# Kernel tuning notes

Measured on AMD Instinct MI355X. Metric: run time of the kernel, lower is better.

## Reference

```python
import jax, jax.numpy as jnp
import numpy as np

B, N, D = 2, 2048, 1024          # batch, query tokens, model dim
NC, DC = 77, 768                 # context tokens, context dim (CLIP)
H, DH = 16, 64                   # heads, head dim (H*DH == D)
FF = 4 * D                       # GEGLU inner dim
SCALE = DH ** -0.5
EPS = 1e-5


def setup_inputs() -> dict:
    key = jax.random.key(0)
    ks = iter(jax.random.split(key, 32))
    rn = lambda *s: jax.random.normal(next(ks), s, dtype=jnp.float32) * 0.02
    inp = {
        'x': jax.random.normal(next(ks), (B, N, D), dtype=jnp.float32),
        'context': jax.random.normal(next(ks), (B, NC, DC), dtype=jnp.float32),
        # attn1 (self-attention): all projections from dim D
        'w1_q': rn(D, D), 'w1_k': rn(D, D), 'w1_v': rn(D, D),
        'w1_o': rn(D, D), 'b1_o': jnp.zeros((D,), jnp.float32),
        # attn2 (cross-attention): k/v from context dim DC
        'w2_q': rn(D, D), 'w2_k': rn(DC, D), 'w2_v': rn(DC, D),
        'w2_o': rn(D, D), 'b2_o': jnp.zeros((D,), jnp.float32),
        # layernorms
        'ln1_g': jnp.ones((D,), jnp.float32), 'ln1_b': jnp.zeros((D,), jnp.float32),
        'ln2_g': jnp.ones((D,), jnp.float32), 'ln2_b': jnp.zeros((D,), jnp.float32),
        'ln3_g': jnp.ones((D,), jnp.float32), 'ln3_b': jnp.zeros((D,), jnp.float32),
        # GEGLU feed-forward: proj -> 2*FF (value, gate), then FF -> D
        'ff_w1': rn(D, 2 * FF), 'ff_b1': jnp.zeros((2 * FF,), jnp.float32),
        'ff_w2': rn(FF, D), 'ff_b2': jnp.zeros((D,), jnp.float32),
    }
    return inp


def _layer_norm(x, g, b):
    mu = jnp.mean(x, axis=-1, keepdims=True)
    var = jnp.mean(jnp.square(x - mu), axis=-1, keepdims=True)
    return (x - mu) * jax.lax.rsqrt(var + EPS) * g + b


def _attention(xq, ctx, wq, wk, wv, wo, bo):
    b, n, _ = xq.shape
    m = ctx.shape[1]
    q = (xq @ wq).reshape(b, n, H, DH)
    k = (ctx @ wk).reshape(b, m, H, DH)
    v = (ctx @ wv).reshape(b, m, H, DH)
    sim = jnp.einsum('bihd,bjhd->bhij', q, k) * SCALE
    attn = jax.nn.softmax(sim, axis=-1)
    out = jnp.einsum('bhij,bjhd->bihd', attn, v).reshape(b, n, H * DH)
    return out @ wo + bo


def reference(x, context,
              w1_q, w1_k, w1_v, w1_o, b1_o,
              w2_q, w2_k, w2_v, w2_o, b2_o,
              ln1_g, ln1_b, ln2_g, ln2_b, ln3_g, ln3_b,
              ff_w1, ff_b1, ff_w2, ff_b2):
    # self-attention + residual
    h = _layer_norm(x, ln1_g, ln1_b)
    x = _attention(h, h, w1_q, w1_k, w1_v, w1_o, b1_o) + x
    # cross-attention + residual
    h = _layer_norm(x, ln2_g, ln2_b)
    x = _attention(h, context, w2_q, w2_k, w2_v, w2_o, b2_o) + x
    # GEGLU feed-forward + residual (torch F.gelu is exact erf)
    h = _layer_norm(x, ln3_g, ln3_b)
    p = h @ ff_w1 + ff_b1
    val, gate = p[..., :FF], p[..., FF:]
    x = (val * jax.nn.gelu(gate, approximate=False)) @ ff_w2 + ff_b2 + x
    return x
```

## Files before the change

kernel.cpp:

```cpp
#include <hip/hip_runtime.h>
#include <hip/hip_bf16.h>
#include <math.h>

#define B_    2
#define N_    2048
#define D_    1024
#define NC_   77
#define DC_   768
#define H_    16
#define DH_   64
#define FF_   4096
#define EPS_  1e-5f
#define SCALE_ 0.125f
#define NEG_BIG -1e30f

typedef __attribute__((ext_vector_type(8))) short short8;
typedef __attribute__((ext_vector_type(4))) float f32x4;
#define MFMA16(a, b, c) __builtin_amdgcn_mfma_f32_16x16x32_bf16(a, b, c, 0, 0, 0)

static __device__ __forceinline__ unsigned short f2bf_raw(float f) {
    union { float f; unsigned int i; } x; x.f = f;
    unsigned int r = x.i + 0x7fffu + ((x.i >> 16) & 1u);
    return (unsigned short)(r >> 16);
}

static __device__ __forceinline__ void gload16(const void* g, void* l) {
    __builtin_amdgcn_global_load_lds(
        (const __attribute__((address_space(1))) void*)g,
        (__attribute__((address_space(3))) void*)l, 16, 0, 0);
}

__global__ __launch_bounds__(256) void wtrans_k(const float* __restrict__ src,
                                                unsigned short* __restrict__ dst,
                                                int K, int N) {
    __shared__ unsigned short t[64][68];
    const int k0 = blockIdx.y * 64, n0 = blockIdx.x * 64;
    const int rr = threadIdx.x >> 4;
    const int cc = (threadIdx.x & 15) * 4;
#pragma unroll
    for (int p = 0; p < 4; p++) {
        int k = rr + p * 16;
        float4 vd = *(const float4*)&src[(size_t)(k0 + k) * N + n0 + cc];
        t[k][cc + 0] = f2bf_raw(vd.x); t[k][cc + 1] = f2bf_raw(vd.y);
        t[k][cc + 2] = f2bf_raw(vd.z); t[k][cc + 3] = f2bf_raw(vd.w);
    }
    __syncthreads();
#pragma unroll
    for (int p = 0; p < 4; p++) {
        int n = rr + p * 16;
        ushort4 o;
        o.x = t[cc + 0][n]; o.y = t[cc + 1][n];
        o.z = t[cc + 2][n]; o.w = t[cc + 3][n];
        *(ushort4*)&dst[(size_t)(n0 + n) * K + k0 + cc] = o;
    }
}

__global__ __launch_bounds__(256) void ln_k(const float* __restrict__ x,
                                            const float* __restrict__ g,
                                            const float* __restrict__ b,
                                            unsigned short* __restrict__ out) {
    int row = blockIdx.x;
    const float* xr = x + (size_t)row * D_;
    float v0[4]; float s = 0.f, sq = 0.f;
#pragma unroll
    for (int i = 0; i < 4; i++) {
        float t = xr[threadIdx.x + 256 * i];
        v0[i] = t; s += t; sq += t * t;
    }
#pragma unroll
    for (int off = 32; off; off >>= 1) {
        s  += __shfl_xor(s,  off);
        sq += __shfl_xor(sq, off);
    }
    __shared__ float rs[4], rq[4];
    int wave = threadIdx.x >> 6, lane = threadIdx.x & 63;
    if (lane == 0) { rs[wave] = s; rq[wave] = sq; }
    __syncthreads();
    s  = rs[0] + rs[1] + rs[2] + rs[3];
    sq = rq[0] + rq[1] + rq[2] + rq[3];
    float mu  = s * (1.f / D_);
    float var = sq * (1.f / D_) - mu * mu;
    float inv = rsqrtf(var + EPS_);
#pragma unroll
    for (int i = 0; i < 4; i++) {
        int c = threadIdx.x + 256 * i;
        out[(size_t)row * D_ + c] = f2bf_raw((v0[i] - mu) * inv * g[c] + b[c]);
    }
}

__global__ __launch_bounds__(256) void gemm_mfma_k(
        const unsigned short* __restrict__ A,
        const unsigned short* __restrict__ BT,
        const float* __restrict__ bias,
        const float* __restrict__ res,
        float* __restrict__ outf,
        unsigned short* __restrict__ oq,
        unsigned short* __restrict__ ok,
        unsigned short* __restrict__ ov,
        int M, int N, int K, int mode) {
    __shared__ unsigned short As[128 * 32];
    __shared__ unsigned short Bs[128 * 32];
    const int tid = threadIdx.x;
    const int w = tid >> 6, lane = tid & 63, quad = lane >> 4, l15 = lane & 15;
    const int wm = w >> 1, wn = w & 1;
    const int m0 = blockIdx.y * 128, n0 = blockIdx.x * 128;
    const int srow = lane >> 2;
    const int schunk = lane & 3;
    const int kswz = (schunk ^ (srow & 3)) * 8;
    const int rdsw = (quad ^ (l15 & 3)) * 8;

    f32x4 acc[4][4] = {};
    for (int k0 = 0; k0 < K; k0 += 32) {
#pragma unroll
        for (int i = 0; i < 2; i++) {
            int r = (w * 2 + i) * 16;
            gload16(&A[(size_t)(m0 + r + srow) * K + k0 + kswz], &As[r * 32]);
            gload16(&BT[(size_t)(n0 + r + srow) * K + k0 + kswz], &Bs[r * 32]);
        }
        __syncthreads();
        short8 af[4], bf[4];
#pragma unroll
        for (int i = 0; i < 4; i++) {
            af[i] = *(const short8*)&As[(wm * 64 + i * 16 + l15) * 32 + rdsw];
            bf[i] = *(const short8*)&Bs[(wn * 64 + i * 16 + l15) * 32 + rdsw];
        }
#pragma unroll
        for (int i = 0; i < 4; i++)
#pragma unroll
            for (int j = 0; j < 4; j++)
                acc[i][j] = MFMA16(af[i], bf[j], acc[i][j]);
        __syncthreads();
    }
#pragma unroll
    for (int i = 0; i < 4; i++) {
#pragma unroll
        for (int r = 0; r < 4; r++) {
            const int row = m0 + wm * 64 + i * 16 + quad * 4 + r;
#pragma unroll
            for (int j = 0; j < 4; j++) {
                const int col = n0 + wn * 64 + j * 16 + l15;
                float c = acc[i][j][r];
                if (mode == 0) {
                    int which = col >> 10, cc = col & 1023;
                    unsigned short* dst = which == 0 ? oq : (which == 1 ? ok : ov);
                    dst[(size_t)row * 1024 + cc] = f2bf_raw(which == 0 ? c * SCALE_ : c);
                } else {
                    outf[(size_t)row * N + col] =
                        c + bias[col] + res[(size_t)row * N + col];
                }
            }
        }
    }
}

__global__ __launch_bounds__(256) void gemm64_k(
        const unsigned short* __restrict__ A,
        const unsigned short* __restrict__ BT,
        const float* __restrict__ bias,
        const float* __restrict__ res,
        float* __restrict__ outf,
        unsigned short* __restrict__ outb,
        float scale,
        int M, int N, int K, int mode) {
    __shared__ unsigned short As[64 * 64];
    __shared__ unsigned short Bs[64 * 64];
    const int tid = threadIdx.x;
    const int w = tid >> 6, lane = tid & 63, quad = lane >> 4, l15 = lane & 15;
    const int wm = w >> 1, wn = w & 1;
    const int m0 = blockIdx.y * 64, n0 = blockIdx.x * 64;
    const int sr8 = lane >> 3;
    const int sc8 = lane & 7;

    f32x4 acc[2][2] = {};
    for (int k0 = 0; k0 < K; k0 += 64) {
#pragma unroll
        for (int i = 0; i < 2; i++) {
            int row = w * 16 + i * 8 + sr8;
            int gch = sc8 ^ (row & 7);
            gload16(&A[(size_t)(m0 + row) * K + k0 + gch * 8], &As[(w * 16 + i * 8) * 64]);
            gload16(&BT[(size_t)(n0 + row) * K + k0 + gch * 8], &Bs[(w * 16 + i * 8) * 64]);
        }
        __syncthreads();
        short8 af[2][2], bf[2][2];
#pragma unroll
        for (int ii = 0; ii < 2; ii++) {
            int ra = wm * 32 + ii * 16 + l15;
            int rb = wn * 32 + ii * 16 + l15;
#pragma unroll
            for (int kh = 0; kh < 2; kh++) {
                int ca = (kh * 4 + quad) ^ (ra & 7);
                int cb = (kh * 4 + quad) ^ (rb & 7);
                af[ii][kh] = *(const short8*)&As[ra * 64 + ca * 8];
                bf[ii][kh] = *(const short8*)&Bs[rb * 64 + cb * 8];
            }
        }
#pragma unroll
        for (int ii = 0; ii < 2; ii++)
#pragma unroll
            for (int jj = 0; jj < 2; jj++) {
                acc[ii][jj] = MFMA16(af[ii][0], bf[jj][0], acc[ii][jj]);
                acc[ii][jj] = MFMA16(af[ii][1], bf[jj][1], acc[ii][jj]);
            }
        __syncthreads();
    }
#pragma unroll
    for (int ii = 0; ii < 2; ii++) {
#pragma unroll
        for (int r = 0; r < 4; r++) {
            const int row = m0 + wm * 32 + ii * 16 + quad * 4 + r;
#pragma unroll
            for (int jj = 0; jj < 2; jj++) {
                const int col = n0 + wn * 32 + jj * 16 + l15;
                float c = acc[ii][jj][r];
                if (mode == 0) {
                    outb[(size_t)row * N + col] = f2bf_raw(c * scale);
                } else {
                    outf[(size_t)row * N + col] =
                        c + bias[col] + res[(size_t)row * N + col];
                }
            }
        }
    }
}

__global__ __launch_bounds__(256, 3) void geglu_mfma_k(
        const unsigned short* __restrict__ A,
        const unsigned short* __restrict__ BT,
        const float* __restrict__ bias,
        unsigned short* __restrict__ outg,
        int M, int K) {
    __shared__ unsigned short As[64 * 32];
    __shared__ unsigned short Bv[128 * 32];
    __shared__ unsigned short Bg[128 * 32];
    const int tid = threadIdx.x;
    const int w = tid >> 6, lane = tid & 63, quad = lane >> 4, l15 = lane & 15;
    const int wm = w >> 1, wn = w & 1;
    const int m0 = blockIdx.y * 64, n0 = blockIdx.x * 128;
    const int srow = lane >> 2;
    const int schunk = lane & 3;
    const int kswz = (schunk ^ (srow & 3)) * 8;
    const int rdsw = (quad ^ (l15 & 3)) * 8;

    f32x4 accv[2][4] = {}, accg[2][4] = {};
    for (int k0 = 0; k0 < K; k0 += 32) {
        gload16(&A[(size_t)(m0 + w * 16 + srow) * K + k0 + kswz],
                &As[(w * 16) * 32]);
#pragma unroll
        for (int i = 0; i < 2; i++) {
            int r = (w * 2 + i) * 16;
            gload16(&BT[(size_t)(n0 + r + srow) * K + k0 + kswz], &Bv[r * 32]);
            gload16(&BT[(size_t)(FF_ + n0 + r + srow) * K + k0 + kswz], &Bg[r * 32]);
        }
        __syncthreads();
        short8 af[2], bvf[4], bgf[4];
#pragma unroll
        for (int i = 0; i < 2; i++)
            af[i]  = *(const short8*)&As[(wm * 32 + i * 16 + l15) * 32 + rdsw];
#pragma unroll
        for (int j = 0; j < 4; j++) {
            bvf[j] = *(const short8*)&Bv[(wn * 64 + j * 16 + l15) * 32 + rdsw];
            bgf[j] = *(const short8*)&Bg[(wn * 64 + j * 16 + l15) * 32 + rdsw];
        }
#pragma unroll
        for (int i = 0; i < 2; i++)
#pragma unroll
            for (int j = 0; j < 4; j++) {
                accv[i][j] = MFMA16(af[i], bvf[j], accv[i][j]);
                accg[i][j] = MFMA16(af[i], bgf[j], accg[i][j]);
            }
        __syncthreads();
    }
#pragma unroll
    for (int i = 0; i < 2; i++) {
#pragma unroll
        for (int r = 0; r < 4; r++) {
            const int row = m0 + wm * 32 + i * 16 + quad * 4 + r;
#pragma unroll
            for (int j = 0; j < 4; j++) {
                const int col = n0 + wn * 64 + j * 16 + l15;
                float vv = accv[i][j][r] + bias[col];
                float gg = accg[i][j][r] + bias[col + FF_];
                float ge = 0.5f * gg * (1.f + erff(gg * 0.70710678118654752f));
                outg[(size_t)row * FF_ + col] = f2bf_raw(vv * ge);
            }
        }
    }
}

__global__ __launch_bounds__(256) void gemm_k(const float* __restrict__ A,
                                              const float* __restrict__ W,
                                              unsigned short* __restrict__ outb,
                                              int M, int N, int K) {
    __shared__ float As[16][64];
    __shared__ float Ws[16][64];
    const int tx = threadIdx.x & 15;
    const int ty = threadIdx.x >> 4;
    const int m0 = blockIdx.y * 64, n0 = blockIdx.x * 64;
    const int lm = threadIdx.x >> 2;
    const int lk = (threadIdx.x & 3) * 4;
    const int wr = threadIdx.x >> 4;
    const int wc = (threadIdx.x & 15) * 4;
    float acc[4][4] = {};
    for (int k0 = 0; k0 < K; k0 += 16) {
        float4 av = make_float4(0.f, 0.f, 0.f, 0.f);
        if (m0 + lm < M) av = *(const float4*)&A[(size_t)(m0 + lm) * K + k0 + lk];
        float4 wv = *(const float4*)&W[(size_t)(k0 + wr) * N + n0 + wc];
        As[lk + 0][lm] = av.x; As[lk + 1][lm] = av.y;
        As[lk + 2][lm] = av.z; As[lk + 3][lm] = av.w;
        *(float4*)&Ws[wr][wc] = wv;
        __syncthreads();
#pragma unroll
        for (int kk = 0; kk < 16; kk++) {
            float4 a = *(const float4*)&As[kk][ty * 4];
            float4 b = *(const float4*)&Ws[kk][tx * 4];
            float ar[4] = { a.x, a.y, a.z, a.w };
            float br[4] = { b.x, b.y, b.z, b.w };
#pragma unroll
            for (int i = 0; i < 4; i++)
#pragma unroll
                for (int j = 0; j < 4; j++)
                    acc[i][j] = fmaf(ar[i], br[j], acc[i][j]);
        }
        __syncthreads();
    }
#pragma unroll
    for (int i = 0; i < 4; i++) {
        int row = m0 + ty * 4 + i;
        if (row >= M) continue;
        ushort4 u;
        u.x = f2bf_raw(acc[i][0]); u.y = f2bf_raw(acc[i][1]);
        u.z = f2bf_raw(acc[i][2]); u.w = f2bf_raw(acc[i][3]);
        *(ushort4*)&outb[(size_t)row * N + n0 + tx * 4] = u;
    }
}

__global__ __launch_bounds__(256) void vtrans_k(const unsigned short* __restrict__ v,
                                                unsigned short* __restrict__ vT,
                                                int ntok, int tokrows, int npad) {
    __shared__ unsigned short tile[64][68];
    const int bh = blockIdx.x, b = bh >> 4, h = bh & 15;
    const int t0 = blockIdx.y * 64;
    const int tt = threadIdx.x >> 4;
    const int dg = (threadIdx.x & 15) * 4;
#pragma unroll
    for (int p = 0; p < 4; p++) {
        int tok = t0 + tt + 16 * p;
        ushort4 val = make_ushort4(0, 0, 0, 0);
        if (tok < ntok)
            val = *(const ushort4*)&v[((size_t)(b * tokrows + tok)) * D_ + h * DH_ + dg];
        *(ushort4*)&tile[tt + 16 * p][dg] = val;
    }
    __syncthreads();
#pragma unroll
    for (int p = 0; p < 4; p++) {
        int d = tt + 16 * p;
        ushort4 w;
        w.x = tile[dg + 0][d]; w.y = tile[dg + 1][d];
        w.z = tile[dg + 2][d]; w.w = tile[dg + 3][d];
        *(ushort4*)&vT[((size_t)(bh * 64 + d)) * npad + t0 + dg] = w;
    }
}

__global__ __launch_bounds__(256, 4) void flash2_k(
        const unsigned short* __restrict__ qb,
        const unsigned short* __restrict__ kb,
        const unsigned short* __restrict__ vT,
        unsigned short* __restrict__ o,
        int n_kv, int kv_rows, int npadv, int ntiles) {
    __shared__ unsigned short Ks[2][64 * 64];
    __shared__ unsigned short Vs[2][64 * 64];
    __shared__ unsigned short Pls[4][16 * 64];
    const int bh = blockIdx.x, b = bh >> 4, h = bh & 15;
    const int w = threadIdx.x >> 6;
    const int lane = threadIdx.x & 63, quad = lane >> 4, l15 = lane & 15;
    const int q0 = blockIdx.y * 64 + w * 16;

    const size_t qoff = ((size_t)(b * N_ + q0 + l15)) * D_ + h * DH_ + quad * 8;
    const short8 qf0 = *(const short8*)&qb[qoff];
    const short8 qf1 = *(const short8*)&qb[qoff + 32];

    short8 onesf;
#pragma unroll
    for (int i = 0; i < 8; i++) onesf[i] = (short)0x3F80;

    const int sr = lane >> 3;
    const int sc = lane & 7;
    const unsigned short* vbase = vT + (size_t)(bh * 64) * npadv;

    auto stage = [&](int buf, int t) {
        const int j0 = t * 64;
#pragma unroll
        for (int i = 0; i < 2; i++) {
            const int row = w * 16 + i * 8 + sr;
            const int gch = (sc ^ (row & 7)) * 8;
            gload16(&kb[(size_t)(b * kv_rows + j0 + row) * D_ + h * DH_ + gch],
                    &Ks[buf][(w * 16 + i * 8) * 64]);
            gload16(&vbase[(size_t)row * npadv + j0 + gch],
                    &Vs[buf][(w * 16 + i * 8) * 64]);
        }
    };

    f32x4 O0 = {0.f, 0.f, 0.f, 0.f}, O1 = O0, O2 = O0, O3 = O0, L4 = O0;
    f32x4 m4 = {NEG_BIG, NEG_BIG, NEG_BIG, NEG_BIG};

    stage(0, 0);
    __syncthreads();

    for (int t = 0; t < ntiles; t++) {
        const int cur = t & 1;
        if (t + 1 < ntiles) stage(cur ^ 1, t + 1);
        const int j0 = t * 64;

        f32x4 s[4];
#pragma unroll
        for (int cb = 0; cb < 4; cb++) {
            const int ra = 16 * cb + l15;
            const int sw = ra & 7;
            const short8 k0 = *(const short8*)&Ks[cur][ra * 64 + ((quad ^ sw) * 8)];
            const short8 k1 = *(const short8*)&Ks[cur][ra * 64 + (((quad + 4) ^ sw) * 8)];
            f32x4 z = {0.f, 0.f, 0.f, 0.f};
            z = MFMA16(qf0, k0, z);
            z = MFMA16(qf1, k1, z);
            s[cb] = z;
        }
        if (j0 + 64 > n_kv) {
#pragma unroll
            for (int cb = 0; cb < 4; cb++)
                if (j0 + 16 * cb + l15 >= n_kv) {
                    s[cb][0] = NEG_BIG; s[cb][1] = NEG_BIG;
                    s[cb][2] = NEG_BIG; s[cb][3] = NEG_BIG;
                }
        }

        f32x4 t4;
#pragma unroll
        for (int r = 0; r < 4; r++)
            t4[r] = fmaxf(fmaxf(s[0][r], s[1][r]), fmaxf(s[2][r], s[3][r]));
#pragma unroll
        for (int off = 1; off < 16; off <<= 1) {
#pragma unroll
            for (int r = 0; r < 4; r++) t4[r] = fmaxf(t4[r], __shfl_xor(t4[r], off));
        }
        f32x4 al;
#pragma unroll
        for (int r = 0; r < 4; r++) {
            float mn = fmaxf(m4[r], t4[r]);
            al[r] = __expf(m4[r] - mn);
            m4[r] = mn;
        }

#pragma unroll
        for (int cb = 0; cb < 4; cb++) {
            const int lc = (l15 >> 3) + 2 * cb;
            const int e = l15 & 7;
#pragma unroll
            for (int r = 0; r < 4; r++) {
                const int pr = quad * 4 + r;
                Pls[w][pr * 64 + ((lc ^ (pr & 7)) * 8 + e)] =
                    f2bf_raw(__expf(s[cb][r] - m4[r]));
            }
        }
#pragma unroll
        for (int r = 0; r < 4; r++) {
            O0[r] *= al[r]; O1[r] *= al[r]; O2[r] *= al[r]; O3[r] *= al[r];
            L4[r] *= al[r];
        }
        const int psw = l15 & 7;
        const short8 pf0 = *(const short8*)&Pls[w][l15 * 64 + ((quad ^ psw) * 8)];
        const short8 pf1 = *(const short8*)&Pls[w][l15 * 64 + (((quad + 4) ^ psw) * 8)];

        short8 vf[4][2];
#pragma unroll
        for (int n = 0; n < 4; n++) {
            const int rv = 16 * n + l15;
            const int vw = rv & 7;
            vf[n][0] = *(const short8*)&Vs[cur][rv * 64 + ((quad ^ vw) * 8)];
            vf[n][1] = *(const short8*)&Vs[cur][rv * 64 + (((quad + 4) ^ vw) * 8)];
        }
        O0 = MFMA16(pf0, vf[0][0], O0); O0 = MFMA16(pf1, vf[0][1], O0);
        O1 = MFMA16(pf0, vf[1][0], O1); O1 = MFMA16(pf1, vf[1][1], O1);
        O2 = MFMA16(pf0, vf[2][0], O2); O2 = MFMA16(pf1, vf[2][1], O2);
        O3 = MFMA16(pf0, vf[3][0], O3); O3 = MFMA16(pf1, vf[3][1], O3);
        L4 = MFMA16(pf0, onesf, L4);    L4 = MFMA16(pf1, onesf, L4);

        __syncthreads();
    }

    const size_t obase = ((size_t)(b * N_ + q0 + quad * 4)) * D_ + h * DH_ + l15;
#pragma unroll
    for (int r = 0; r < 4; r++) {
        const float inv = 1.0f / L4[r];
        unsigned short* orow = &o[obase + (size_t)r * D_];
        orow[0]  = f2bf_raw(O0[r] * inv);
        orow[16] = f2bf_raw(O1[r] * inv);
        orow[32] = f2bf_raw(O2[r] * inv);
        orow[48] = f2bf_raw(O3[r] * inv);
    }
}

extern "C" void kernel_launch(void* const* d_in, const int* in_sizes, int n_in,
                              void* d_out, int out_size, void* d_ws, size_t ws_size,
                              hipStream_t stream) {
    const float* x_in  = (const float*)d_in[0];
    const float* ctx_in= (const float*)d_in[1];
    const float* w1q = (const float*)d_in[2];
    const float* w1k = (const float*)d_in[3];
    const float* w1v = (const float*)d_in[4];
    const float* w1o = (const float*)d_in[5];
    const float* b1o = (const float*)d_in[6];
    const float* w2q = (const float*)d_in[7];
    const float* w2k = (const float*)d_in[8];
    const float* w2v = (const float*)d_in[9];
    const float* w2o = (const float*)d_in[10];
    const float* b2o = (const float*)d_in[11];
    const float* ln1g= (const float*)d_in[12];
    const float* ln1b= (const float*)d_in[13];
    const float* ln2g= (const float*)d_in[14];
    const float* ln2b= (const float*)d_in[15];
    const float* ln3g= (const float*)d_in[16];
    const float* ln3b= (const float*)d_in[17];
    const float* ffw1= (const float*)d_in[18];
    const float* ffb1= (const float*)d_in[19];
    const float* ffw2= (const float*)d_in[20];
    const float* ffb2= (const float*)d_in[21];
    float* out_f = (float*)d_out;

    char* ws = (char*)d_ws;
    unsigned short* wqkvT = (unsigned short*)(ws);
    unsigned short* w1oT  = (unsigned short*)(ws + (size_t)( 6 << 20));
    unsigned short* w2qT  = (unsigned short*)(ws + (size_t)( 8 << 20));
    unsigned short* w2oT  = (unsigned short*)(ws + (size_t)(10 << 20));
    unsigned short* ffw1T = (unsigned short*)(ws + (size_t)(12 << 20));
    unsigned short* ffw2T = (unsigned short*)(ws + (size_t)(28 << 20));
    float*          xbuf  = (float*)         (ws + (size_t)(36 << 20));
    unsigned short* h     = (unsigned short*)(ws + (size_t)(52 << 20));
    unsigned short* qb    = (unsigned short*)(ws + (size_t)(60 << 20));
    unsigned short* kb    = (unsigned short*)(ws + (size_t)(68 << 20));
    unsigned short* vTb   = (unsigned short*)(ws + (size_t)(76 << 20));
    unsigned short* vb    = (unsigned short*)(ws + (size_t)(84 << 20));
    unsigned short* g     = (unsigned short*)(ws + (size_t)(60 << 20));

    const int MT = B_ * N_;

    auto wt = [&](const float* src, unsigned short* dst, int K, int N) {
        hipLaunchKernelGGL(wtrans_k, dim3(N / 64, K / 64), dim3(256), 0, stream, src, dst, K, N);
    };
    auto gmm = [&](const unsigned short* A, const unsigned short* BT,
                   const float* bias, const float* res, float* outf,
                   unsigned short* oq, unsigned short* ok, unsigned short* ov,
                   int M, int N, int K, int mode) {
        hipLaunchKernelGGL(gemm_mfma_k, dim3(N / 128, M / 128), dim3(256), 0, stream,
                           A, BT, bias, res, outf, oq, ok, ov, M, N, K, mode);
    };
    auto g64 = [&](const unsigned short* A, const unsigned short* BT,
                   const float* bias, const float* res, float* outf,
                   unsigned short* outb, float scale, int M, int N, int K, int mode) {
        hipLaunchKernelGGL(gemm64_k, dim3(N / 64, M / 64), dim3(256), 0, stream,
                           A, BT, bias, res, outf, outb, scale, M, N, K, mode);
    };

    wt(w1q, wqkvT,                 D_, D_);
    wt(w1k, wqkvT + (1024 * 1024), D_, D_);
    wt(w1v, wqkvT + (2048 * 1024), D_, D_);
    wt(w1o, w1oT, D_, D_);
    wt(w2q, w2qT, D_, D_);
    wt(w2o, w2oT, D_, D_);
    wt(ffw1, ffw1T, D_, 2 * FF_);
    wt(ffw2, ffw2T, FF_, D_);

    hipLaunchKernelGGL(ln_k, dim3(MT), dim3(256), 0, stream, x_in, ln1g, ln1b, h);
    gmm(h, wqkvT, nullptr, nullptr, nullptr, qb, kb, vb, MT, 3072, D_, 0);
    hipLaunchKernelGGL(vtrans_k, dim3(B_ * H_, N_ / 64), dim3(256), 0, stream,
                       vb, vTb, N_, N_, N_);
    hipLaunchKernelGGL(flash2_k, dim3(B_ * H_, N_ / 64), dim3(256), 0, stream,
                       qb, kb, vTb, vb , N_, N_, N_, N_ / 64);
    g64(vb , w1oT, b1o, x_in, xbuf, nullptr, 1.0f, MT, D_, D_, 1);

    hipLaunchKernelGGL(ln_k, dim3(MT), dim3(256), 0, stream, xbuf, ln2g, ln2b, h);
    g64(h, w2qT, nullptr, nullptr, nullptr, qb, SCALE_, MT, D_, D_, 0);
    hipLaunchKernelGGL(gemm_k, dim3(D_ / 64, 3), dim3(256), 0, stream,
                       ctx_in, w2k, kb, B_ * NC_, D_, DC_);
    hipLaunchKernelGGL(gemm_k, dim3(D_ / 64, 3), dim3(256), 0, stream,
                       ctx_in, w2v, vb, B_ * NC_, D_, DC_);
    hipLaunchKernelGGL(vtrans_k, dim3(B_ * H_, 2), dim3(256), 0, stream,
                       vb, vTb, NC_, NC_, 128);
    hipLaunchKernelGGL(flash2_k, dim3(B_ * H_, N_ / 64), dim3(256), 0, stream,
                       qb, kb, vTb, vb , NC_, NC_, 128, 2);
    g64(vb , w2oT, b2o, xbuf, xbuf, nullptr, 1.0f, MT, D_, D_, 1);

    hipLaunchKernelGGL(ln_k, dim3(MT), dim3(256), 0, stream, xbuf, ln3g, ln3b, h);
    hipLaunchKernelGGL(geglu_mfma_k, dim3(FF_ / 128, MT / 64), dim3(256), 0, stream,
                       h, ffw1T, ffb1, g, MT, D_);
    g64(g, ffw2T, ffb2, xbuf, out_f, nullptr, 1.0f, MT, D_, FF_, 1);
}
```

Measured before the change: 652.8 us.

## Deepen GEGLU GEMM K-tile to 64 and reorganize warp tiling

```diff
diff --git a/kernel.cpp b/kernel.cpp
--- a/kernel.cpp
+++ b/kernel.cpp
@@ -223,63 +223,75 @@
     }
 }
 
-__global__ __launch_bounds__(256, 3) void geglu_mfma_k(
+__global__ __launch_bounds__(256, 4) void geglu_mfma_k(
         const unsigned short* __restrict__ A,
         const unsigned short* __restrict__ BT,
         const float* __restrict__ bias,
         unsigned short* __restrict__ outg,
         int M, int K) {
-    __shared__ unsigned short As[64 * 32];
-    __shared__ unsigned short Bv[128 * 32];
-    __shared__ unsigned short Bg[128 * 32];
+    __shared__ unsigned short As[64 * 64];
+    __shared__ unsigned short Bv[128 * 64];
+    __shared__ unsigned short Bg[128 * 64];
     const int tid = threadIdx.x;
     const int w = tid >> 6, lane = tid & 63, quad = lane >> 4, l15 = lane & 15;
-    const int wm = w >> 1, wn = w & 1;
     const int m0 = blockIdx.y * 64, n0 = blockIdx.x * 128;
-    const int srow = lane >> 2;
-    const int schunk = lane & 3;
-    const int kswz = (schunk ^ (srow & 3)) * 8;
-    const int rdsw = (quad ^ (l15 & 3)) * 8;
-
-    f32x4 accv[2][4] = {}, accg[2][4] = {};
-    for (int k0 = 0; k0 < K; k0 += 32) {
-        gload16(&A[(size_t)(m0 + w * 16 + srow) * K + k0 + kswz],
-                &As[(w * 16) * 32]);
+    const int sr8 = lane >> 3, sc8 = lane & 7;
+
+    f32x4 accv[4][2] = {}, accg[4][2] = {};
+    for (int k0 = 0; k0 < K; k0 += 64) {
 #pragma unroll
         for (int i = 0; i < 2; i++) {
-            int r = (w * 2 + i) * 16;
-            gload16(&BT[(size_t)(n0 + r + srow) * K + k0 + kswz], &Bv[r * 32]);
-            gload16(&BT[(size_t)(FF_ + n0 + r + srow) * K + k0 + kswz], &Bg[r * 32]);
-        }
-        __syncthreads();
-        short8 af[2], bvf[4], bgf[4];
-#pragma unroll
-        for (int i = 0; i < 2; i++)
-            af[i]  = *(const short8*)&As[(wm * 32 + i * 16 + l15) * 32 + rdsw];
-#pragma unroll
-        for (int j = 0; j < 4; j++) {
-            bvf[j] = *(const short8*)&Bv[(wn * 64 + j * 16 + l15) * 32 + rdsw];
-            bgf[j] = *(const short8*)&Bg[(wn * 64 + j * 16 + l15) * 32 + rdsw];
-        }
-#pragma unroll
-        for (int i = 0; i < 2; i++)
-#pragma unroll
-            for (int j = 0; j < 4; j++) {
-                accv[i][j] = MFMA16(af[i], bvf[j], accv[i][j]);
-                accg[i][j] = MFMA16(af[i], bgf[j], accg[i][j]);
-            }
-        __syncthreads();
-    }
-#pragma unroll
-    for (int i = 0; i < 2; i++) {
+            int row = w * 16 + i * 8 + sr8;
+            int gch = sc8 ^ (row & 7);
+            gload16(&A[(size_t)(m0 + row) * K + k0 + gch * 8], &As[(w * 16 + i * 8) * 64]);
+        }
+#pragma unroll
+        for (int i = 0; i < 4; i++) {
+            int row = w * 32 + i * 8 + sr8;
+            int gch = sc8 ^ (row & 7);
+            gload16(&BT[(size_t)(n0 + row) * K + k0 + gch * 8], &Bv[(w * 32 + i * 8) * 64]);
+            gload16(&BT[(size_t)(FF_ + n0 + row) * K + k0 + gch * 8], &Bg[(w * 32 + i * 8) * 64]);
+        }
+        __syncthreads();
+        short8 af[4][2];
+#pragma unroll
+        for (int ii = 0; ii < 4; ii++) {
+            int ra = ii * 16 + l15;
+#pragma unroll
+            for (int kh = 0; kh < 2; kh++) {
+                int ca = (kh * 4 + quad) ^ (ra & 7);
+                af[ii][kh] = *(const short8*)&As[ra * 64 + ca * 8];
+            }
+        }
+#pragma unroll
+        for (int jj = 0; jj < 2; jj++) {
+            const int rb = w * 32 + jj * 16 + l15;
+            const int c0 = (0 * 4 + quad) ^ (rb & 7);
+            const int c1 = (1 * 4 + quad) ^ (rb & 7);
+            const short8 bv0 = *(const short8*)&Bv[rb * 64 + c0 * 8];
+            const short8 bv1 = *(const short8*)&Bv[rb * 64 + c1 * 8];
+            const short8 bg0 = *(const short8*)&Bg[rb * 64 + c0 * 8];
+            const short8 bg1 = *(const short8*)&Bg[rb * 64 + c1 * 8];
+#pragma unroll
+            for (int ii = 0; ii < 4; ii++) {
+                accv[ii][jj] = MFMA16(af[ii][0], bv0, accv[ii][jj]);
+                accv[ii][jj] = MFMA16(af[ii][1], bv1, accv[ii][jj]);
+                accg[ii][jj] = MFMA16(af[ii][0], bg0, accg[ii][jj]);
+                accg[ii][jj] = MFMA16(af[ii][1], bg1, accg[ii][jj]);
+            }
+        }
+        __syncthreads();
+    }
+#pragma unroll
+    for (int ii = 0; ii < 4; ii++) {
 #pragma unroll
         for (int r = 0; r < 4; r++) {
-            const int row = m0 + wm * 32 + i * 16 + quad * 4 + r;
-#pragma unroll
-            for (int j = 0; j < 4; j++) {
-                const int col = n0 + wn * 64 + j * 16 + l15;
-                float vv = accv[i][j][r] + bias[col];
-                float gg = accg[i][j][r] + bias[col + FF_];
+            const int row = m0 + ii * 16 + quad * 4 + r;
+#pragma unroll
+            for (int jj = 0; jj < 2; jj++) {
+                const int col = n0 + w * 32 + jj * 16 + l15;
+                float vv = accv[ii][jj][r] + bias[col];
+                float gg = accg[ii][jj][r] + bias[col + FF_];
                 float ge = 0.5f * gg * (1.f + erff(gg * 0.70710678118654752f));
                 outg[(size_t)row * FF_ + col] = f2bf_raw(vv * ge);
             }
```

Measured after the change: 645.0 us. About the same (-1.2%).
